# Optimization experiments

Measured on AMD Instinct MI355X. Metric: run time of the kernel, lower is better.

The kernel has to match this reference:

```python
import jax, jax.numpy as jnp
import numpy as np

N = 100_000      # nodes
E = 3_200_000    # edges (avg degree 32)
NF = 16          # node_features
SF = 32          # second_features
NC = 10          # num_classes


def setup_inputs() -> dict:
    key = jax.random.key(0)
    ks = jax.random.split(key, 16)
    s_in = 1.0 / np.sqrt(NF)
    s_g = 1.0 / np.sqrt(2 * SF)
    s_o = 1.0 / np.sqrt(SF)
    return {
        "x": jax.random.normal(ks[0], (N, NF), jnp.float32),
        "edge_index": jax.random.randint(ks[1], (2, E), 0, N, dtype=jnp.int32),
        "edge_weight": jax.random.uniform(ks[2], (E,), jnp.float32, 0.1, 1.0),
        # GCNConv weights for z / r / h gates (in->out) + biases
        "Wz": jax.random.normal(ks[3], (NF, SF), jnp.float32) * s_in,
        "bz": jnp.zeros((SF,), jnp.float32),
        "Wr": jax.random.normal(ks[4], (NF, SF), jnp.float32) * s_in,
        "br": jnp.zeros((SF,), jnp.float32),
        "Wh": jax.random.normal(ks[5], (NF, SF), jnp.float32) * s_in,
        "bh": jnp.zeros((SF,), jnp.float32),
        # gate linears: Linear(2*SF -> SF)
        "Lz_W": jax.random.normal(ks[6], (2 * SF, SF), jnp.float32) * s_g,
        "Lz_b": jnp.zeros((SF,), jnp.float32),
        "Lr_W": jax.random.normal(ks[7], (2 * SF, SF), jnp.float32) * s_g,
        "Lr_b": jnp.zeros((SF,), jnp.float32),
        "Lh_W": jax.random.normal(ks[8], (2 * SF, SF), jnp.float32) * s_g,
        "Lh_b": jnp.zeros((SF,), jnp.float32),
        # final classifier Linear(SF -> NC)
        "out_W": jax.random.normal(ks[9], (SF, NC), jnp.float32) * s_o,
        "out_b": jnp.zeros((NC,), jnp.float32),
        # A3TGCN temporal attention over periods=1 (softmax -> 1.0)
        "attention": jax.random.uniform(ks[10], (1,), jnp.float32),
    }


def _gcn_norm(edge_index, edge_weight, n):
    # PyG gcn_norm with add_self_loops=True, fill_value=1.0
    row, col = edge_index[0], edge_index[1]
    loop = jnp.arange(n, dtype=edge_index.dtype)
    row = jnp.concatenate([row, loop])
    col = jnp.concatenate([col, loop])
    w = jnp.concatenate([edge_weight, jnp.ones((n,), edge_weight.dtype)])
    deg = jax.ops.segment_sum(w, col, num_segments=n)
    dinv = jnp.where(deg > 0, jax.lax.rsqrt(deg), 0.0)
    return row, col, dinv[row] * w * dinv[col]


def _gcn(x, W, b, row, col, norm, n):
    xw = x @ W                                        # [N, SF]
    agg = jax.ops.segment_sum(xw[row] * norm[:, None], col, num_segments=n)
    return agg + b


def reference(x, edge_index, edge_weight, Wz, bz, Wr, br, Wh, bh,
              Lz_W, Lz_b, Lr_W, Lr_b, Lh_W, Lh_b, out_W, out_b, attention):
    n = x.shape[0]
    row, col, norm = _gcn_norm(edge_index, edge_weight, n)
    H0 = jnp.zeros((n, SF), x.dtype)                  # initial hidden state
    # TGCN GRU cell (single step, periods=1)
    Z = jax.nn.sigmoid(jnp.concatenate([_gcn(x, Wz, bz, row, col, norm, n), H0], 1) @ Lz_W + Lz_b)
    R = jax.nn.sigmoid(jnp.concatenate([_gcn(x, Wr, br, row, col, norm, n), H0], 1) @ Lr_W + Lr_b)
    H_tilde = jnp.tanh(jnp.concatenate([_gcn(x, Wh, bh, row, col, norm, n), H0 * R], 1) @ Lh_W + Lh_b)
    H = Z * H0 + (1.0 - Z) * H_tilde
    # A3TGCN attention-weighted temporal pooling (periods=1 -> weight 1.0)
    H = jax.nn.softmax(attention)[0] * H
    h = jax.nn.relu(H)
    logits = h @ out_W + out_b
    return jax.nn.softmax(logits, axis=1)
```

## Files before the change

### kernel.cpp

```cpp
#include <hip/hip_runtime.h>

#define NF 16
#define SF 32
#define NC 10
#define MAXDEG 96
#define BSH 7
#define BCAP 4608
#define ECHUNK 8192

__device__ __forceinline__ unsigned pack_bf2(float a, float b) {
    unsigned ua = __float_as_uint(a), ub = __float_as_uint(b);
    ua = (ua + 0x7fffu + ((ua >> 16) & 1u)) >> 16;
    ub = (ub + 0x7fffu + ((ub >> 16) & 1u)) >> 16;
    return ua | (ub << 16);
}
__device__ __forceinline__ float bf_lo(unsigned u) { return __uint_as_float(u << 16); }
__device__ __forceinline__ float bf_hi(unsigned u) { return __uint_as_float(u & 0xffff0000u); }

__global__ void k_zero(int* __restrict__ p, int n) {
    int i = blockIdx.x * blockDim.x + threadIdx.x;
    if (i < n) p[i] = 0;
}

__global__ void k_precomp(const float* __restrict__ Wz, const float* __restrict__ Wh,
                          const float* __restrict__ bz, const float* __restrict__ bh,
                          const float* __restrict__ LzW, const float* __restrict__ Lzb,
                          const float* __restrict__ LhW, const float* __restrict__ Lhb,
                          float* __restrict__ Wzl, float* __restrict__ Whl,
                          float* __restrict__ bzl, float* __restrict__ bhl) {
    int t = threadIdx.x;
    int m = t >> 5, jo = t & 31;
    float sz = 0.0f, sh = 0.0f;
    for (int jm = 0; jm < SF; ++jm) {
        sz += Wz[m * SF + jm] * LzW[jm * SF + jo];
        sh += Wh[m * SF + jm] * LhW[jm * SF + jo];
    }
    Wzl[m * SF + jo] = sz;
    Whl[m * SF + jo] = sh;
    if (t < SF) {
        float az = Lzb[t], ah = Lhb[t];
        for (int jm = 0; jm < SF; ++jm) {
            az += bz[jm] * LzW[jm * SF + t];
            ah += bh[jm] * LhW[jm * SF + t];
        }
        bzl[t] = az; bhl[t] = ah;
    }
}

__global__ __launch_bounds__(512) void k_bucket(
    const int* __restrict__ row, const int* __restrict__ col,
    const float* __restrict__ w, int* __restrict__ bucket_cnt,
    unsigned* __restrict__ bbuf, int E, int NB) {
    __shared__ unsigned sorted[ECHUNK];
    __shared__ unsigned short bs[ECHUNK];
    __shared__ int hist[1024];
    __shared__ int boff[1024];
    __shared__ int off[1024];
    __shared__ int gbase[1024];
    int t = threadIdx.x;
    hist[t] = 0; hist[t + 512] = 0;
    __syncthreads();

    long e0 = (long)blockIdx.x * ECHUNK;
    long rem = (long)E - e0;
    int cnt = (rem < ECHUNK) ? (int)(rem < 0 ? 0 : rem) : ECHUNK;

    unsigned lo[16];
    int bb[16];
#pragma unroll
    for (int r = 0; r < 16; ++r) {
        int i = t + r * 512;
        lo[r] = 0; bb[r] = 0;
        if (i < cnt) {
            long e = e0 + i;
            int c = col[e];
            unsigned w8 = (unsigned)__float2int_rn(w[e] * 255.0f);
            lo[r] = ((unsigned)row[e] << 15) | ((unsigned)(c & 127) << 8) | w8;
            int b = c >> BSH;
            bb[r] = b;
            atomicAdd(&hist[b], 1);
        }
    }
    __syncthreads();

    int h0 = hist[t], h1 = hist[t + 512];
    boff[t] = h0; boff[t + 512] = h1;
    __syncthreads();
    for (int o = 1; o < 1024; o <<= 1) {
        int a0 = (t >= o) ? boff[t - o] : 0;
        int a1 = (t + 512 >= o) ? boff[t + 512 - o] : 0;
        __syncthreads();
        boff[t] += a0; boff[t + 512] += a1;
        __syncthreads();
    }
    boff[t] -= h0; boff[t + 512] -= h1;
    __syncthreads();

    for (int b = t; b < NB; b += 512) {
        int h = hist[b];
        off[b] = 0;
        int basel = h ? atomicAdd(&bucket_cnt[b], h) : 0;
        if (basel > BCAP) basel = BCAP;
        gbase[b] = b * BCAP + basel - boff[b];
    }
    __syncthreads();

#pragma unroll
    for (int r = 0; r < 16; ++r) {
        int i = t + r * 512;
        if (i < cnt) {
            int b = bb[r];
            int p = atomicAdd(&off[b], 1);
            int pos = boff[b] + p;
            sorted[pos] = lo[r];
            bs[pos] = (unsigned short)b;
        }
    }
    __syncthreads();

#pragma unroll
    for (int r = 0; r < 16; ++r) {
        int i = t + r * 512;
        if (i < cnt) {
            int b = bs[i];
            int dst = gbase[b] + i;
            if (dst < (b + 1) * BCAP)
                bbuf[(size_t)dst] = sorted[i];
        }
    }
}

__global__ __launch_bounds__(256) void k_build(
    const int* __restrict__ bucket_cnt, const unsigned* __restrict__ bbuf,
    const float* __restrict__ x,
    unsigned* __restrict__ csr, int* __restrict__ count,
    float* __restrict__ dinv, unsigned* __restrict__ y, int N) {
    __shared__ unsigned clds[BCAP];
    __shared__ int comb[128];
    __shared__ int loff[128];
    __shared__ int lcur[128];
    __shared__ int sscan[128];
    __shared__ float sdinv[128];
    int t = threadIdx.x;
    if (t < 128) { comb[t] = 0; lcur[t] = 0; }
    __syncthreads();
    int b = blockIdx.x;
    int cnt = bucket_cnt[b]; if (cnt > BCAP) cnt = BCAP;
    const unsigned* src = bbuf + (size_t)b * BCAP;

    for (int i = t; i < cnt; i += 256) {
        unsigned v = src[i];
        int cl = (int)((v >> 8) & 127u);
        atomicAdd(&comb[cl], 0x10000 | (int)(v & 0xFFu));
    }
    __syncthreads();
    int sv = 0;
    if (t < 128) { sv = comb[t] >> 16; sscan[t] = sv; }
    __syncthreads();
    for (int o = 1; o < 128; o <<= 1) {
        int add = (t >= o && t < 128) ? sscan[t - o] : 0;
        __syncthreads();
        if (t < 128) sscan[t] += add;
        __syncthreads();
    }
    if (t < 128) {
        loff[t] = sscan[t] - sv;
        int g = b * 128 + t;
        if (g < N) {
            int c = sv; if (c > MAXDEG) c = MAXDEG;
            count[g] = c;
            float dv = rsqrtf(1.0f + (float)(comb[t] & 0xFFFF) * (1.0f / 255.0f));
            dinv[g] = dv;
            sdinv[t] = dv;
        }
    }
    __syncthreads();
    for (int i = t; i < cnt; i += 256) {
        unsigned v = src[i];
        int cl = (int)((v >> 8) & 127u);
        int p = atomicAdd(&lcur[cl], 1);
        clds[loff[cl] + p] = ((v >> 7) & 0xFFFFFF00u) | (v & 0xFFu);
    }
    __syncthreads();
    int wv = t >> 6, ln = t & 63;
    for (int i = wv; i < 128; i += 4) {
        int gg = b * 128 + i;
        if (gg >= N) break;
        int c = comb[i] >> 16; if (c > MAXDEG) c = MAXDEG;
        int base = loff[i];
        for (int p = ln; p < c; p += 64)
            csr[(size_t)gg * MAXDEG + p] = clds[base + p];
    }
    for (int idx = t; idx < 128 * 8; idx += 256) {
        int i = idx >> 3, fl = idx & 7;
        int gg = b * 128 + i;
        if (gg < N) {
            float2 xv = ((const float2*)x)[(size_t)gg * 8 + fl];
            float di = sdinv[i];
            y[(size_t)gg * 8 + fl] = pack_bf2(di * xv.x, di * xv.y);
        }
    }
}

__global__ __launch_bounds__(256) void k_gather(
    const unsigned* __restrict__ y, const float* __restrict__ dinv,
    const int* __restrict__ count, const unsigned* __restrict__ csr,
    float* __restrict__ uout, int N) {
    int t = threadIdx.x;
    int l    = t & 63;
    int half = l & 32;
    int hl   = l & 31;
    int eg   = hl >> 3;
    int fl   = hl & 7;
    int sub  = eg << 3;
    int ghw  = (blockIdx.x * 256 + t) >> 5;
    int nhw  = gridDim.x * 8;
    const char* ybase = (const char*)y + (fl << 2);
    float selfsel = (eg == 0) ? 255.0f : 0.0f;

    int nA = ghw, nB = nA + nhw;
    int   cntA = 0, cntB = 0;
    float diA = 0.0f;
    unsigned eA0 = 0, eA1 = 0, eA2 = 0, svA = 0;
    if (nA < N) cntA = count[nA];
    if (nB < N) cntB = count[nB];
    if (nA < N) {
        diA = dinv[nA];
        const unsigned* cb = csr + (size_t)nA * MAXDEG;
        if (hl < cntA)      eA0 = cb[hl];
        if (32 + hl < cntA) eA1 = cb[32 + hl];
        if (64 + hl < cntA) eA2 = cb[64 + hl];
        svA = y[(size_t)nA * 8 + fl];
    }

    for (int n = nA; n < N; n += nhw) {
        int nn  = n + nhw;
        int nnn = nn + nhw;
        int cntC = (nnn < N) ? count[nnn] : 0;
        float diB = 0.0f;
        unsigned eB0 = 0, eB1 = 0, eB2 = 0, svB = 0;
        if (nn < N) {
            diB = dinv[nn];
            const unsigned* cb = csr + (size_t)nn * MAXDEG;
            if (hl < cntB)      eB0 = cb[hl];
            if (32 + hl < cntB) eB1 = cb[32 + hl];
            if (64 + hl < cntB) eB2 = cb[64 + hl];
            svB = y[(size_t)nn * 8 + fl];
        }

        float a0 = selfsel * bf_lo(svA);
        float a1 = selfsel * bf_hi(svA);
#define BLK(E0, EDR)                                                             \
        if ((E0) < cntA) {                                                       \
            unsigned se[8]; unsigned g[8];                                       \
            _Pragma("unroll")                                                    \
            for (int r = 0; r < 8; ++r)                                          \
                se[r] = (unsigned)__shfl((int)(EDR), half + sub + r, 64);        \
            _Pragma("unroll")                                                    \
            for (int r = 0; r < 8; ++r)                                          \
                g[r] = *(const unsigned*)(ybase + ((se[r] >> 3) & 0xFFFFFFE0u)); \
            _Pragma("unroll")                                                    \
            for (int r = 0; r < 8; ++r) {                                        \
                float wf = (float)(se[r] & 0xFFu);                               \
                a0 = fmaf(bf_lo(g[r]), wf, a0);                                  \
                a1 = fmaf(bf_hi(g[r]), wf, a1);                                  \
            }                                                                    \
        }
        BLK(0, eA0)
        BLK(32, eA1)
        BLK(64, eA2)
#undef BLK
        a0 += __shfl_xor(a0, 8, 64);  a0 += __shfl_xor(a0, 16, 64);
        a1 += __shfl_xor(a1, 8, 64);  a1 += __shfl_xor(a1, 16, 64);

        if (eg == 0) {
            float s = diA * (1.0f / 255.0f);
            ((float2*)uout)[(size_t)n * 8 + fl] = make_float2(a0 * s, a1 * s);
        }

        cntA = cntB; cntB = cntC;
        diA = diB;
        eA0 = eB0; eA1 = eB1; eA2 = eB2;
        svA = svB;
    }
}

__global__ __launch_bounds__(256) void k_epi(
    const float* __restrict__ u,
    const float* __restrict__ Wzl, const float* __restrict__ Whl,
    const float* __restrict__ bzl, const float* __restrict__ bhl,
    const float* __restrict__ oW, const float* __restrict__ ob,
    float* __restrict__ out, int N) {
    int t = threadIdx.x;
    int l = t & 63, half = l & 32, hl = l & 31;

    const float* msel = (hl < 16) ? Wzl : Whl;
    const float* bsel = (hl < 16) ? bzl : bhl;
    int c0 = (2 * hl) & 31;
    float mc0[NF], mc1[NF];
#pragma unroll
    for (int k = 0; k < NF; ++k) {
        mc0[k] = msel[k * SF + c0];
        mc1[k] = msel[k * SF + c0 + 1];
    }
    float b0 = bsel[c0], b1 = bsel[c0 + 1];
    int c = (hl < NC) ? hl : (NC - 1);
    float ow[SF];
#pragma unroll
    for (int j = 0; j < SF; ++j) ow[j] = oW[j * NC + c];
    float obv = ob[c];

    int ghw = (blockIdx.x * 256 + t) >> 5;
    int nhw = gridDim.x * 8;
    for (int n = ghw; n < N; n += nhw) {
        const float4* u4 = (const float4*)(u + (size_t)n * 16);
        float4 ua = u4[0], ub = u4[1], uc = u4[2], ud = u4[3];
        float uu[16] = {ua.x, ua.y, ua.z, ua.w, ub.x, ub.y, ub.z, ub.w,
                        uc.x, uc.y, uc.z, uc.w, ud.x, ud.y, ud.z, ud.w};
        float v0 = b0, v1 = b1;
#pragma unroll
        for (int k = 0; k < NF; ++k) {
            v0 = fmaf(uu[k], mc0[k], v0);
            v1 = fmaf(uu[k], mc1[k], v1);
        }
        if (hl < 16) { v0 = 1.0f / (1.0f + expf(-v0)); v1 = 1.0f / (1.0f + expf(-v1)); }
        else         { v0 = tanhf(v0);                  v1 = tanhf(v1); }
        int pl = half + ((hl + 16) & 31);
        float w0 = __shfl(v0, pl, 64);
        float w1 = __shfl(v1, pl, 64);
        float h0 = fmaxf((1.0f - v0) * w0, 0.0f);
        float h1 = fmaxf((1.0f - v1) * w1, 0.0f);

        float lg = obv;
#pragma unroll
        for (int j = 0; j < SF; ++j) {
            float hv = __shfl((j & 1) ? h1 : h0, half + (j >> 1), 64);
            lg = fmaf(hv, ow[j], lg);
        }
        lg = (hl < NC) ? lg : -1e30f;
        float mx = lg;
#pragma unroll
        for (int m = 1; m < 16; m <<= 1) mx = fmaxf(mx, __shfl_xor(mx, m, 64));
        float ex = expf(lg - mx);
        float ss = ex;
#pragma unroll
        for (int m = 1; m < 16; m <<= 1) ss += __shfl_xor(ss, m, 64);
        if (hl < NC) out[(size_t)n * NC + hl] = ex / ss;
    }
}

extern "C" void kernel_launch(void* const* d_in, const int* in_sizes, int n_in,
                              void* d_out, int out_size, void* d_ws, size_t ws_size,
                              hipStream_t stream) {
    const float* x   = (const float*)d_in[0];
    const int*   ei  = (const int*)d_in[1];
    const float* ew  = (const float*)d_in[2];
    const float* Wz  = (const float*)d_in[3];
    const float* bz  = (const float*)d_in[4];
    const float* Wh  = (const float*)d_in[7];
    const float* bh  = (const float*)d_in[8];
    const float* LzW = (const float*)d_in[9];
    const float* Lzb = (const float*)d_in[10];
    const float* LhW = (const float*)d_in[13];
    const float* Lhb = (const float*)d_in[14];
    const float* oW  = (const float*)d_in[15];
    const float* ob  = (const float*)d_in[16];
    float* out = (float*)d_out;

    int N = in_sizes[0] / NF;
    int E = in_sizes[2];
    const int* row = ei;
    const int* col = ei + E;
    int NB = (N + 127) >> 7;

    char* p = (char*)d_ws;
    auto alloc = [&](size_t bytes) {
        char* r = p;
        p += (bytes + 255) & ~(size_t)255;
        return r;
    };
    int*      bucket_cnt = (int*)alloc((size_t)NB * 4);
    int*      count      = (int*)alloc((size_t)N * 4);
    float*    dinv       = (float*)alloc((size_t)N * 4);
    unsigned* y          = (unsigned*)alloc((size_t)N * 8 * 4);
    float*    u          = (float*)alloc((size_t)N * 16 * 4);
    unsigned* csr        = (unsigned*)alloc((size_t)N * MAXDEG * 4);
    unsigned* bbuf       = (unsigned*)alloc((size_t)NB * BCAP * 4);
    float*    Wzl        = (float*)alloc(NF * SF * 4);
    float*    Whl        = (float*)alloc(NF * SF * 4);
    float*    bzl        = (float*)alloc(SF * 4);
    float*    bhl        = (float*)alloc(SF * 4);

    k_zero<<<(NB + 255) / 256, 256, 0, stream>>>(bucket_cnt, NB);
    k_precomp<<<1, 512, 0, stream>>>(Wz, Wh, bz, bh, LzW, Lzb, LhW, Lhb,
                                     Wzl, Whl, bzl, bhl);
    k_bucket<<<(E + ECHUNK - 1) / ECHUNK, 512, 0, stream>>>(row, col, ew,
                                                            bucket_cnt, bbuf, E, NB);
    k_build<<<NB, 256, 0, stream>>>(bucket_cnt, bbuf, x, csr, count, dinv, y, N);
    k_gather<<<2048, 256, 0, stream>>>(y, dinv, count, csr, u, N);
    k_epi<<<2048, 256, 0, stream>>>(u, Wzl, Whl, bzl, bhl, oW, ob, out, N);
}
```

Before: 111.9 us.

## Replace LDS scans with wave-shuffle scan and single-pass fixed-slot CSR build

In the bucketing kernel, the 1024-entry Hillis-Steele LDS scan, which needs many barriers, is replaced by a per-wave shuffle scan over bucket pairs plus a small cross-wave total. The CSR build kernel drops its separate counting pass and 128-entry scan. Edges now go directly into fixed MAXDEG slots per node in LDS, and the weighted degree and dinv are computed during the copy-out with a wave reduction. The k_zero launch is replaced with hipMemsetAsync. The trade-offs are a larger LDS footprint in k_build, which may lower occupancy, and a degree sum that counts only the first MAXDEG edges of each node.

```diff
diff --git a/kernel.cpp b/kernel.cpp
--- a/kernel.cpp
+++ b/kernel.cpp
@@ -17,11 +17,6 @@
 __device__ __forceinline__ float bf_lo(unsigned u) { return __uint_as_float(u << 16); }
 __device__ __forceinline__ float bf_hi(unsigned u) { return __uint_as_float(u & 0xffff0000u); }
 
-__global__ void k_zero(int* __restrict__ p, int n) {
-    int i = blockIdx.x * blockDim.x + threadIdx.x;
-    if (i < n) p[i] = 0;
-}
-
 __global__ void k_precomp(const float* __restrict__ Wz, const float* __restrict__ Wh,
                           const float* __restrict__ bz, const float* __restrict__ bh,
                           const float* __restrict__ LzW, const float* __restrict__ Lzb,
@@ -54,11 +49,13 @@
     __shared__ unsigned sorted[ECHUNK];
     __shared__ unsigned short bs[ECHUNK];
     __shared__ int hist[1024];
-    __shared__ int boff[1024];
+    __shared__ int boffs[1024];
     __shared__ int off[1024];
     __shared__ int gbase[1024];
+    __shared__ int wtot[8];
     int t = threadIdx.x;
     hist[t] = 0; hist[t + 512] = 0;
+    off[t] = 0;  off[t + 512] = 0;
     __syncthreads();
 
     long e0 = (long)blockIdx.x * ECHUNK;
@@ -83,25 +80,33 @@
     }
     __syncthreads();
 
-    int h0 = hist[t], h1 = hist[t + 512];
-    boff[t] = h0; boff[t + 512] = h1;
-    __syncthreads();
-    for (int o = 1; o < 1024; o <<= 1) {
-        int a0 = (t >= o) ? boff[t - o] : 0;
-        int a1 = (t + 512 >= o) ? boff[t + 512 - o] : 0;
-        __syncthreads();
-        boff[t] += a0; boff[t + 512] += a1;
-        __syncthreads();
-    }
-    boff[t] -= h0; boff[t + 512] -= h1;
-    __syncthreads();
-
-    for (int b = t; b < NB; b += 512) {
-        int h = hist[b];
-        off[b] = 0;
-        int basel = h ? atomicAdd(&bucket_cnt[b], h) : 0;
+    int lane = t & 63, wv = t >> 6;
+    int h0 = hist[2 * t], h1 = hist[2 * t + 1];
+    int pair = h0 + h1;
+    int incl = pair;
+#pragma unroll
+    for (int d = 1; d < 64; d <<= 1) {
+        int v = __shfl_up(incl, d, 64);
+        if (lane >= d) incl += v;
+    }
+    if (lane == 63) wtot[wv] = incl;
+    __syncthreads();
+    int wbase = 0;
+#pragma unroll
+    for (int k = 0; k < 8; ++k) wbase += (k < wv) ? wtot[k] : 0;
+    int excl = wbase + incl - pair;
+    boffs[2 * t] = excl;
+    boffs[2 * t + 1] = excl + h0;
+    int b0 = 2 * t, b1 = 2 * t + 1;
+    if (b0 < NB) {
+        int basel = h0 ? atomicAdd(&bucket_cnt[b0], h0) : 0;
         if (basel > BCAP) basel = BCAP;
-        gbase[b] = b * BCAP + basel - boff[b];
+        gbase[b0] = b0 * BCAP + basel - excl;
+    }
+    if (b1 < NB) {
+        int basel = h1 ? atomicAdd(&bucket_cnt[b1], h1) : 0;
+        if (basel > BCAP) basel = BCAP;
+        gbase[b1] = b1 * BCAP + basel - (excl + h0);
     }
     __syncthreads();
 
@@ -111,7 +116,7 @@
         if (i < cnt) {
             int b = bb[r];
             int p = atomicAdd(&off[b], 1);
-            int pos = boff[b] + p;
+            int pos = boffs[b] + p;
             sorted[pos] = lo[r];
             bs[pos] = (unsigned short)b;
         }
@@ -135,62 +140,45 @@
     const float* __restrict__ x,
     unsigned* __restrict__ csr, int* __restrict__ count,
     float* __restrict__ dinv, unsigned* __restrict__ y, int N) {
-    __shared__ unsigned clds[BCAP];
-    __shared__ int comb[128];
-    __shared__ int loff[128];
+    __shared__ unsigned clds[128 * MAXDEG];
     __shared__ int lcur[128];
-    __shared__ int sscan[128];
     __shared__ float sdinv[128];
     int t = threadIdx.x;
-    if (t < 128) { comb[t] = 0; lcur[t] = 0; }
+    if (t < 128) lcur[t] = 0;
     __syncthreads();
     int b = blockIdx.x;
     int cnt = bucket_cnt[b]; if (cnt > BCAP) cnt = BCAP;
     const unsigned* src = bbuf + (size_t)b * BCAP;
 
-    for (int i = t; i < cnt; i += 256) {
-        unsigned v = src[i];
-        int cl = (int)((v >> 8) & 127u);
-        atomicAdd(&comb[cl], 0x10000 | (int)(v & 0xFFu));
-    }
-    __syncthreads();
-    int sv = 0;
-    if (t < 128) { sv = comb[t] >> 16; sscan[t] = sv; }
-    __syncthreads();
-    for (int o = 1; o < 128; o <<= 1) {
-        int add = (t >= o && t < 128) ? sscan[t - o] : 0;
-        __syncthreads();
-        if (t < 128) sscan[t] += add;
-        __syncthreads();
-    }
-    if (t < 128) {
-        loff[t] = sscan[t] - sv;
-        int g = b * 128 + t;
-        if (g < N) {
-            int c = sv; if (c > MAXDEG) c = MAXDEG;
-            count[g] = c;
-            float dv = rsqrtf(1.0f + (float)(comb[t] & 0xFFFF) * (1.0f / 255.0f));
-            dinv[g] = dv;
-            sdinv[t] = dv;
-        }
-    }
-    __syncthreads();
     for (int i = t; i < cnt; i += 256) {
         unsigned v = src[i];
         int cl = (int)((v >> 8) & 127u);
         int p = atomicAdd(&lcur[cl], 1);
-        clds[loff[cl] + p] = ((v >> 7) & 0xFFFFFF00u) | (v & 0xFFu);
+        if (p < MAXDEG)
+            clds[cl * MAXDEG + p] = ((v >> 7) & 0xFFFFFF00u) | (v & 0xFFu);
     }
     __syncthreads();
     int wv = t >> 6, ln = t & 63;
     for (int i = wv; i < 128; i += 4) {
         int gg = b * 128 + i;
         if (gg >= N) break;
-        int c = comb[i] >> 16; if (c > MAXDEG) c = MAXDEG;
-        int base = loff[i];
-        for (int p = ln; p < c; p += 64)
-            csr[(size_t)gg * MAXDEG + p] = clds[base + p];
-    }
+        int c = lcur[i]; if (c > MAXDEG) c = MAXDEG;
+        float s = 0.0f;
+        for (int p = ln; p < c; p += 64) {
+            unsigned v = clds[i * MAXDEG + p];
+            csr[(size_t)gg * MAXDEG + p] = v;
+            s += (float)(v & 0xFFu);
+        }
+#pragma unroll
+        for (int m = 1; m < 64; m <<= 1) s += __shfl_xor(s, m, 64);
+        if (ln == 0) {
+            count[gg] = c;
+            float dv = rsqrtf(1.0f + s * (1.0f / 255.0f));
+            dinv[gg] = dv;
+            sdinv[i] = dv;
+        }
+    }
+    __syncthreads();
     for (int idx = t; idx < 128 * 8; idx += 256) {
         int i = idx >> 3, fl = idx & 7;
         int gg = b * 128 + i;
@@ -391,7 +379,7 @@
     float*    bzl        = (float*)alloc(SF * 4);
     float*    bhl        = (float*)alloc(SF * 4);
 
-    k_zero<<<(NB + 255) / 256, 256, 0, stream>>>(bucket_cnt, NB);
+    hipMemsetAsync(bucket_cnt, 0, (size_t)NB * 4, stream);
     k_precomp<<<1, 512, 0, stream>>>(Wz, Wh, bz, bh, LzW, Lzb, LhW, Lhb,
                                      Wzl, Whl, bzl, bhl);
     k_bucket<<<(E + ECHUNK - 1) / ECHUNK, 512, 0, stream>>>(row, col, ew,
```

After: 143.7 us. 28.5% more time.
